# Kernel optimization log

Measured on AMD Instinct MI355X. Metric: run time of the kernel, lower is better.

## Reference

```python
import jax, jax.numpy as jnp
import numpy as np

B, C, U, V, H, W = 4, 64, 5, 5, 64, 64
MID = 64  # mid_dim defaults to dim


def setup_inputs() -> dict:
    key = jax.random.key(0)
    ks = jax.random.split(key, 13)
    s = 0.05
    inp = {"x": jax.random.normal(ks[0], (B, C, U, V, H, W), dtype=jnp.float32)}
    # body: Conv2d(dim->mid,1x1), SiLU, Conv2d(mid->dim,1x1)
    inp["w1"] = jax.random.normal(ks[1], (MID, C), dtype=jnp.float32) * s
    inp["b1"] = jax.random.normal(ks[2], (MID,), dtype=jnp.float32) * s
    inp["w2"] = jax.random.normal(ks[3], (C, MID), dtype=jnp.float32) * s
    inp["b2"] = jax.random.normal(ks[4], (C,), dtype=jnp.float32) * s
    # four fuse 1x1 convs (dim->dim)
    for i in range(4):
        inp[f"fw{i}"] = jax.random.normal(ks[5 + 2 * i], (C, C), dtype=jnp.float32) * s
        inp[f"fb{i}"] = jax.random.normal(ks[6 + 2 * i], (C,), dtype=jnp.float32) * s
    return inp


def _conv1x1(w, b, x):
    # x: (B,C,h,w); w: (O,C); 1x1 conv == channel matmul
    return jnp.einsum('oc,bchw->bohw', w, x) + b[None, :, None, None]


def reference(x, w1, b1, w2, b2, fw0, fb0, fw1, fb1, fw2, fb2, fw3, fb3):
    # Four 2-axis mean pools over the 6D tensor
    hw_m = x.mean(axis=(2, 3))   # (B,C,H,W)
    uv_m = x.mean(axis=(4, 5))   # (B,C,U,V)
    uh_m = x.mean(axis=(3, 5))   # (B,C,U,H)
    vw_m = x.mean(axis=(2, 4))   # (B,C,V,W)
    # Assemble padded buffer uvhw of shape (B,C,H+V,W+U)
    top = jnp.concatenate([hw_m, jnp.swapaxes(uh_m, -1, -2)], axis=-1)  # (B,C,H,W+U)
    bot = jnp.concatenate([vw_m, jnp.swapaxes(uv_m, -1, -2)], axis=-1)  # (B,C,V,W+U)
    uvhw = jnpp_concat = jnp.concatenate([top, bot], axis=-2)           # (B,C,H+V,W+U)
    # body: conv1x1 -> SiLU -> conv1x1
    uvhw = _conv1x1(w2, b2, jax.nn.silu(_conv1x1(w1, b1, uvhw)))
    # Split back into the four pooled maps
    hw = uvhw[..., :H, :W]
    vw = uvhw[..., H:, :W]
    uh = jnp.swapaxes(uvhw[..., :H, W:], -1, -2)  # (B,C,U,H)
    uv = jnp.swapaxes(uvhw[..., H:, W:], -1, -2)  # (B,C,U,V)
    # Per-branch fuse convs, then broadcast-gate x and sum
    hw = _conv1x1(fw0, fb0, hw).reshape(B, C, 1, 1, H, W)
    uv = _conv1x1(fw1, fb1, uv).reshape(B, C, U, V, 1, 1)
    uh = _conv1x1(fw2, fb2, uh).reshape(B, C, U, 1, H, 1)
    vw = _conv1x1(fw3, fb3, vw).reshape(B, C, 1, V, 1, W)
    return x * hw + x * uv + x * uh + x * vw
```

## Files before the change

kernel.cpp:

```cpp
#include <hip/hip_runtime.h>
#include <hip/hip_bf16.h>
#include <cstddef>

#define BB 4
#define CC 64
#define UU 5
#define VV 5
#define HH 64
#define WW 64

typedef float f4v __attribute__((ext_vector_type(4)));

__device__ __forceinline__ float rdlane(float v, int l) {
    return __uint_as_float((unsigned)__builtin_amdgcn_readlane((int)__float_as_uint(v), l));
}
__device__ __forceinline__ float rfl(float v) {
    return __uint_as_float((unsigned)__builtin_amdgcn_readfirstlane((int)__float_as_uint(v)));
}
__device__ __forceinline__ float sum4(float4 a) { return (a.x+a.y)+(a.z+a.w); }
__device__ __forceinline__ void nt_store4(float4 r, float4* p) {
    union { float4 s; f4v v; } u; u.s = r;
    __builtin_nontemporal_store(u.v, (f4v*)p);
}

__global__ __launch_bounds__(512) void k1_means(const float* __restrict__ x,
        float* __restrict__ m_hw, float* __restrict__ R,
        float* __restrict__ vw_part) {
    const int bid  = blockIdx.x;
    const int bc   = bid >> 1;
    const int half = bid & 1;
    const int t    = threadIdx.x;
    const int p    = half*512 + t;
    const int wave = t >> 6;
    const int lane = t & 63;

    const float4* xt = (const float4*)x + (size_t)bc * 25600;

    __shared__ float smem[25*512];

    float4 hw = make_float4(0.f,0.f,0.f,0.f);
    float4 vwacc[5];
    #pragma unroll
    for (int v = 0; v < 5; ++v) vwacc[v] = make_float4(0.f,0.f,0.f,0.f);

    #pragma unroll
    for (int u = 0; u < 5; ++u) {
        #pragma unroll
        for (int v = 0; v < 5; ++v) {
            float4 q = xt[(u*5 + v)*1024 + p];
            hw.x += q.x; hw.y += q.y; hw.z += q.z; hw.w += q.w;
            vwacc[v].x += q.x; vwacc[v].y += q.y;
            vwacc[v].z += q.z; vwacc[v].w += q.w;
            smem[(u*5 + v)*512 + t] = sum4(q);
        }
    }

    float4 o;
    o.x = hw.x*(1.f/25.f); o.y = hw.y*(1.f/25.f);
    o.z = hw.z*(1.f/25.f); o.w = hw.w*(1.f/25.f);
    ((float4*)m_hw)[(size_t)bc*1024 + p] = o;

    __syncthreads();

    for (int task = t; task < 800; task += 512) {
        const int k    = task >> 5;
        const int hloc = task & 31;
        const float* row = &smem[k*512 + hloc*16];
        float s = 0.f;
        #pragma unroll
        for (int j = 0; j < 16; ++j) s += row[j];
        R[((size_t)bc*25 + k)*64 + half*32 + hloc] = s;
    }
    __syncthreads();

    float4* vwbuf = (float4*)smem;
    #pragma unroll
    for (int v = 0; v < 5; ++v) {
        float4 s = vwacc[v];
        s.x += __shfl_xor(s.x, 16); s.y += __shfl_xor(s.y, 16);
        s.z += __shfl_xor(s.z, 16); s.w += __shfl_xor(s.w, 16);
        s.x += __shfl_xor(s.x, 32); s.y += __shfl_xor(s.y, 32);
        s.z += __shfl_xor(s.z, 32); s.w += __shfl_xor(s.w, 32);
        if (lane < 16) vwbuf[(wave*5 + v)*16 + lane] = s;
    }
    __syncthreads();

    if (t < 80) {
        const int v = t >> 4;
        float4 s = vwbuf[(0*5 + v)*16 + (t & 15)];
        #pragma unroll
        for (int w8 = 1; w8 < 8; ++w8) {
            float4 pp = vwbuf[(w8*5 + v)*16 + (t & 15)];
            s.x += pp.x; s.y += pp.y; s.z += pp.z; s.w += pp.w;
        }
        ((float4*)vw_part)[(size_t)bid*80 + t] = s;
    }
}

#define LOADROW(dst, src)                                              \
    { _Pragma("unroll")                                                \
      for (int q = 0; q < 16; ++q) {                                   \
          float4 t4 = ((const float4*)(src))[lane*16 + q];             \
          dst[4*q+0] = t4.x; dst[4*q+1] = t4.y;                        \
          dst[4*q+2] = t4.z; dst[4*q+3] = t4.w;                        \
      } }

#define DOT64(res, wr, src)                                            \
    float res;                                                         \
    { float _a0=0.f,_a1=0.f,_a2=0.f,_a3=0.f;                           \
      _Pragma("unroll")                                                \
      for (int cc2 = 0; cc2 < 64; cc2 += 4) {                          \
          _a0 = fmaf(wr[cc2+0], rdlane(src, cc2+0), _a0);              \
          _a1 = fmaf(wr[cc2+1], rdlane(src, cc2+1), _a1);              \
          _a2 = fmaf(wr[cc2+2], rdlane(src, cc2+2), _a2);              \
          _a3 = fmaf(wr[cc2+3], rdlane(src, cc2+3), _a3);              \
      }                                                                \
      res = (_a0 + _a1) + (_a2 + _a3); }

#define MLP_CORE(VIN, OUTEXPR)                                         \
    {                                                                  \
        float v = (VIN);                                               \
        DOT64(d1, w1r, v);                                             \
        float acc1 = d1 + b1v;                                         \
        float ya = acc1 / (1.f + __expf(-acc1));                       \
        DOT64(d2, w2r, ya);                                            \
        float acc2 = d2 + b2v;                                         \
        DOT64(d3, fr, acc2);                                           \
        OUTEXPR = d3 + fbv;                                            \
    }

__global__ __launch_bounds__(64, 1) void k2_mlp(
        const float* __restrict__ m_hw, const float* __restrict__ R,
        const float* __restrict__ vw_part,
        const float* __restrict__ w1, const float* __restrict__ b1,
        const float* __restrict__ w2, const float* __restrict__ b2,
        const float* __restrict__ fw0, const float* __restrict__ fb0,
        const float* __restrict__ fw1, const float* __restrict__ fb1,
        const float* __restrict__ fw2, const float* __restrict__ fb2,
        const float* __restrict__ fw3, const float* __restrict__ fb3,
        float* __restrict__ mod_hw, float* __restrict__ mod_uh,
        float* __restrict__ mod_vw, float* __restrict__ mod_uv) {
    const int blk  = blockIdx.x;
    const int row  = blk >> 2;
    const int chnk = blk & 3;
    const int b    = row / 69;
    const int i    = row % 69;
    const int lane = threadIdx.x & 63;

    const int j0 = chnk * 18;
    const int j1 = min(69, j0 + 18);
    const bool top = (i < 64);

    const float* fwA = top ? fw0 : fw3;
    const float* fbA = top ? fb0 : fb3;
    const float* fwB = top ? fw2 : fw1;
    const float* fbB = top ? fb2 : fb1;

    float w1r[64], w2r[64], fr[64];
    LOADROW(w1r, w1);
    LOADROW(w2r, w2);
    const float b1v = b1[lane];
    const float b2v = b2[lane];

    const int b64c = b * CC + lane;
    const int cbl  = b64c;

    const int jm = min(j1, 64);
    if (j0 < jm) {
        LOADROW(fr, fwA);
        const float fbv = fbA[lane];
        if (top) {
            const float* src = m_hw + (size_t)b64c*4096 + i*64;
            float* sp = mod_hw + ((size_t)cbl*64 + i)*64;
            for (int j = j0; j < jm; ++j)
                MLP_CORE(src[j], sp[j])
        } else {
            const float* p0 = vw_part + (size_t)b64c*640 + (i-64)*64;
            const float* q0 = vw_part + ((size_t)b64c*2 + 0)*320 + (i-64)*64;
            const float* q1 = vw_part + ((size_t)b64c*2 + 1)*320 + (i-64)*64;
            float* sp = mod_vw + (size_t)cbl*320 + (i-64)*64;
            (void)p0;
            for (int j = j0; j < jm; ++j)
                MLP_CORE((q0[j] + q1[j]) * (1.f/320.f), sp[j])
        }
    }
    if (j1 > 64) {
        LOADROW(fr, fwB);
        const float fbv = fbB[lane];
        const int jb = max(j0, 64);
        if (top) {
            float* sp = mod_uh + (size_t)cbl*320 + i;
            for (int j = jb; j < j1; ++j) {
                const int u = j - 64;
                const float* Rp = R + ((size_t)b64c*25 + u*5)*64 + i;
                float vin = (Rp[0] + Rp[64] + Rp[128] + Rp[192] + Rp[256])
                            * (1.f/320.f);
                MLP_CORE(vin, sp[(size_t)u*64])
            }
        } else {
            float* sp = mod_uv + (size_t)cbl*25 + (i-64);
            for (int j = jb; j < j1; ++j) {
                const int u = j - 64;
                const float4* Rp4 = (const float4*)(R
                    + ((size_t)b64c*25 + u*5 + (i-64))*64);
                float4 a = make_float4(0.f,0.f,0.f,0.f);
                #pragma unroll
                for (int k = 0; k < 16; ++k) {
                    float4 pp = Rp4[k];
                    a.x += pp.x; a.y += pp.y; a.z += pp.z; a.w += pp.w;
                }
                MLP_CORE(sum4(a) * (1.f/4096.f), sp[(size_t)u*5])
            }
        }
    }
}

__global__ __launch_bounds__(256, 4) void k3_apply(
        const float* __restrict__ x,
        const float* __restrict__ mod_hw, const float* __restrict__ mod_uh,
        const float* __restrict__ mod_vw, const float* __restrict__ mod_uv,
        float* __restrict__ out) {
    const int blk  = blockIdx.x;
    const int bc   = blk >> 2;
    const int qt   = blk & 3;
    const int t    = threadIdx.x;
    const int base = qt*256 + t;
    const int h    = base >> 4;

    float4 mh = ((const float4*)(mod_hw + (size_t)bc * 4096))[base];
    float uh[5];
    #pragma unroll
    for (int u = 0; u < 5; ++u) uh[u] = mod_uh[(size_t)bc*320 + u*64 + h];
    float4 vw[5];
    #pragma unroll
    for (int v = 0; v < 5; ++v)
        vw[v] = ((const float4*)(mod_vw + (size_t)bc*320 + v*64))[t & 15];
    float uv[25];
    #pragma unroll
    for (int k = 0; k < 25; ++k)
        uv[k] = rfl(mod_uv[(size_t)bc*25 + k]);

    const float4* x4 = (const float4*)(x + (size_t)bc * (UU*VV*HH*WW));
    float4* o4 = (float4*)(out + (size_t)bc * (UU*VV*HH*WW));

    #pragma unroll
    for (int u = 0; u < 5; ++u) {
        #pragma unroll
        for (int v = 0; v < 5; ++v) {
            const int idx = (u*5 + v)*1024 + base;
            float4 xv = x4[idx];
            const float s = uh[u] + uv[u*5 + v];
            float4 r;
            r.x = xv.x * (mh.x + vw[v].x + s);
            r.y = xv.y * (mh.y + vw[v].y + s);
            r.z = xv.z * (mh.z + vw[v].z + s);
            r.w = xv.w * (mh.w + vw[v].w + s);
            nt_store4(r, &o4[idx]);
        }
    }
}

extern "C" void kernel_launch(void* const* d_in, const int* in_sizes, int n_in,
                              void* d_out, int out_size, void* d_ws, size_t ws_size,
                              hipStream_t stream) {
    const float* x   = (const float*)d_in[0];
    const float* w1  = (const float*)d_in[1];
    const float* b1  = (const float*)d_in[2];
    const float* w2  = (const float*)d_in[3];
    const float* b2  = (const float*)d_in[4];
    const float* fw0 = (const float*)d_in[5];
    const float* fb0 = (const float*)d_in[6];
    const float* fw1 = (const float*)d_in[7];
    const float* fb1 = (const float*)d_in[8];
    const float* fw2 = (const float*)d_in[9];
    const float* fb2 = (const float*)d_in[10];
    const float* fw3 = (const float*)d_in[11];
    const float* fb3 = (const float*)d_in[12];

    float* ws = (float*)d_ws;
    float* mod_hw = ws;
    float* mod_uh = mod_hw + 1048576;
    float* mod_vw = mod_uh + 81920;
    float* mod_uv = mod_vw + 81920;

    float* m_hw    = (float*)d_out;
    float* Rbuf    = m_hw + 1048576;
    float* vw_part = Rbuf + 409600;

    k1_means<<<BB*CC*2, 512, 0, stream>>>(x, m_hw, Rbuf, vw_part);
    k2_mlp<<<BB*69*4, 64, 0, stream>>>(m_hw, Rbuf, vw_part, w1, b1, w2, b2,
                                       fw0, fb0, fw1, fb1, fw2, fb2, fw3, fb3,
                                       mod_hw, mod_uh, mod_vw, mod_uv);
    k3_apply<<<BB*CC*4, 256, 0, stream>>>(x, mod_hw, mod_uh, mod_vw, mod_uv,
                                          (float*)d_out);
}
```

Measured before the change: 100.4 us.

## Split k1 means reduction across U slices and finish hw/vw sums in k2

```diff
diff --git a/kernel.cpp b/kernel.cpp
--- a/kernel.cpp
+++ b/kernel.cpp
@@ -23,53 +23,53 @@
     __builtin_nontemporal_store(u.v, (f4v*)p);
 }
 
-__global__ __launch_bounds__(512) void k1_means(const float* __restrict__ x,
-        float* __restrict__ m_hw, float* __restrict__ R,
+__global__ __launch_bounds__(256) void k1_means(const float* __restrict__ x,
+        float* __restrict__ part_hw, float* __restrict__ R,
         float* __restrict__ vw_part) {
-    const int bid  = blockIdx.x;
-    const int bc   = bid >> 1;
-    const int half = bid & 1;
+    const int bid = blockIdx.x;
+    const int bc  = bid / 5;
+    const int u   = bid % 5;
     const int t    = threadIdx.x;
-    const int p    = half*512 + t;
     const int wave = t >> 6;
     const int lane = t & 63;
 
-    const float4* xt = (const float4*)x + (size_t)bc * 25600;
-
-    __shared__ float smem[25*512];
-
-    float4 hw = make_float4(0.f,0.f,0.f,0.f);
+    const float4* xs = (const float4*)x + (size_t)bc * 25600 + (size_t)u * 5120;
+
+    __shared__ float smem[5*1024];
+
+    float4 hwacc[4];
+    #pragma unroll
+    for (int r = 0; r < 4; ++r) hwacc[r] = make_float4(0.f,0.f,0.f,0.f);
     float4 vwacc[5];
     #pragma unroll
     for (int v = 0; v < 5; ++v) vwacc[v] = make_float4(0.f,0.f,0.f,0.f);
 
     #pragma unroll
-    for (int u = 0; u < 5; ++u) {
-        #pragma unroll
-        for (int v = 0; v < 5; ++v) {
-            float4 q = xt[(u*5 + v)*1024 + p];
-            hw.x += q.x; hw.y += q.y; hw.z += q.z; hw.w += q.w;
+    for (int v = 0; v < 5; ++v) {
+        #pragma unroll
+        for (int r = 0; r < 4; ++r) {
+            float4 q = xs[(v*4 + r)*256 + t];
+            hwacc[r].x += q.x; hwacc[r].y += q.y;
+            hwacc[r].z += q.z; hwacc[r].w += q.w;
             vwacc[v].x += q.x; vwacc[v].y += q.y;
             vwacc[v].z += q.z; vwacc[v].w += q.w;
-            smem[(u*5 + v)*512 + t] = sum4(q);
-        }
-    }
-
-    float4 o;
-    o.x = hw.x*(1.f/25.f); o.y = hw.y*(1.f/25.f);
-    o.z = hw.z*(1.f/25.f); o.w = hw.w*(1.f/25.f);
-    ((float4*)m_hw)[(size_t)bc*1024 + p] = o;
+            smem[v*1024 + r*256 + t] = sum4(q);
+        }
+    }
+
+    #pragma unroll
+    for (int r = 0; r < 4; ++r)
+        ((float4*)part_hw)[(size_t)bid*1024 + r*256 + t] = hwacc[r];
 
     __syncthreads();
 
-    for (int task = t; task < 800; task += 512) {
-        const int k    = task >> 5;
-        const int hloc = task & 31;
-        const float* row = &smem[k*512 + hloc*16];
+    for (int task = t; task < 320; task += 256) {
+        const int v = task >> 6, h = task & 63;
+        const float* row = &smem[v*1024 + h*16];
         float s = 0.f;
         #pragma unroll
         for (int j = 0; j < 16; ++j) s += row[j];
-        R[((size_t)bc*25 + k)*64 + half*32 + hloc] = s;
+        R[((size_t)bc*25 + u*5 + v)*64 + h] = s;
     }
     __syncthreads();
 
@@ -89,8 +89,8 @@
         const int v = t >> 4;
         float4 s = vwbuf[(0*5 + v)*16 + (t & 15)];
         #pragma unroll
-        for (int w8 = 1; w8 < 8; ++w8) {
-            float4 pp = vwbuf[(w8*5 + v)*16 + (t & 15)];
+        for (int w4 = 1; w4 < 4; ++w4) {
+            float4 pp = vwbuf[(w4*5 + v)*16 + (t & 15)];
             s.x += pp.x; s.y += pp.y; s.z += pp.z; s.w += pp.w;
         }
         ((float4*)vw_part)[(size_t)bid*80 + t] = s;
@@ -130,7 +130,7 @@
     }
 
 __global__ __launch_bounds__(64, 1) void k2_mlp(
-        const float* __restrict__ m_hw, const float* __restrict__ R,
+        const float* __restrict__ part_hw, const float* __restrict__ R,
         const float* __restrict__ vw_part,
         const float* __restrict__ w1, const float* __restrict__ b1,
         const float* __restrict__ w2, const float* __restrict__ b2,
@@ -170,18 +170,21 @@
         LOADROW(fr, fwA);
         const float fbv = fbA[lane];
         if (top) {
-            const float* src = m_hw + (size_t)b64c*4096 + i*64;
+            const float* ph = part_hw + (size_t)b64c*5*4096 + i*64;
             float* sp = mod_hw + ((size_t)cbl*64 + i)*64;
-            for (int j = j0; j < jm; ++j)
-                MLP_CORE(src[j], sp[j])
+            for (int j = j0; j < jm; ++j) {
+                float vin = (((ph[j] + ph[4096 + j]) + (ph[2*4096 + j]
+                           + ph[3*4096 + j])) + ph[4*4096 + j]) * (1.f/25.f);
+                MLP_CORE(vin, sp[j])
+            }
         } else {
-            const float* p0 = vw_part + (size_t)b64c*640 + (i-64)*64;
-            const float* q0 = vw_part + ((size_t)b64c*2 + 0)*320 + (i-64)*64;
-            const float* q1 = vw_part + ((size_t)b64c*2 + 1)*320 + (i-64)*64;
+            const float* pv = vw_part + (size_t)b64c*5*320 + (i-64)*64;
             float* sp = mod_vw + (size_t)cbl*320 + (i-64)*64;
-            (void)p0;
-            for (int j = j0; j < jm; ++j)
-                MLP_CORE((q0[j] + q1[j]) * (1.f/320.f), sp[j])
+            for (int j = j0; j < jm; ++j) {
+                float vin = (((pv[j] + pv[320 + j]) + (pv[2*320 + j]
+                           + pv[3*320 + j])) + pv[4*320 + j]) * (1.f/320.f);
+                MLP_CORE(vin, sp[j])
+            }
         }
     }
     if (j1 > 64) {
@@ -283,12 +286,12 @@
     float* mod_vw = mod_uh + 81920;
     float* mod_uv = mod_vw + 81920;
 
-    float* m_hw    = (float*)d_out;
-    float* Rbuf    = m_hw + 1048576;
+    float* part_hw = (float*)d_out;
+    float* Rbuf    = part_hw + 5242880;
     float* vw_part = Rbuf + 409600;
 
-    k1_means<<<BB*CC*2, 512, 0, stream>>>(x, m_hw, Rbuf, vw_part);
-    k2_mlp<<<BB*69*4, 64, 0, stream>>>(m_hw, Rbuf, vw_part, w1, b1, w2, b2,
+    k1_means<<<BB*CC*UU, 256, 0, stream>>>(x, part_hw, Rbuf, vw_part);
+    k2_mlp<<<BB*69*4, 64, 0, stream>>>(part_hw, Rbuf, vw_part, w1, b1, w2, b2,
                                        fw0, fb0, fw1, fb1, fw2, fb2, fw3, fb3,
                                        mod_hw, mod_uh, mod_vw, mod_uv);
     k3_apply<<<BB*CC*4, 256, 0, stream>>>(x, mod_hw, mod_uh, mod_vw, mod_uv,
```

New measurement: 195.8 us. 95.0% more time.
